# Kernel optimization log

Hardware: AMD Instinct MI355X
Metric: run time of the kernel (lower is better)

## Reference

```python
import jax, jax.numpy as jnp
import numpy as np

B = 2
T = 1024
D_MODEL = 1024
EXPAND = 2
D_INNER = D_MODEL * EXPAND  # 2048
D_STATE = 16
D_CONV = 4
DT_RANK = 64  # ceil(1024/16)


def setup_inputs() -> dict:
    key = jax.random.key(0)
    ks = jax.random.split(key, 9)
    s = 0.02
    x = jax.random.normal(ks[0], (B, T, D_MODEL), jnp.float32)
    in_proj_w = jax.random.normal(ks[1], (2 * D_INNER, D_MODEL), jnp.float32) * s
    conv_w = jax.random.normal(ks[2], (D_INNER, 1, D_CONV), jnp.float32) * 0.1
    conv_b = jax.random.normal(ks[3], (D_INNER,), jnp.float32) * 0.01
    x_proj_w = jax.random.normal(ks[4], (DT_RANK + 2 * D_STATE, D_INNER), jnp.float32) * s
    dt_proj_w = jax.random.normal(ks[5], (D_INNER, DT_RANK), jnp.float32) * s
    dt_proj_b = jax.random.uniform(ks[6], (D_INNER,), jnp.float32, -4.0, -2.0)
    A_log = jnp.log(jnp.tile(jnp.arange(1, D_STATE + 1, dtype=jnp.float32), (D_INNER, 1)))
    D_param = jnp.ones((D_INNER,), jnp.float32)
    out_proj_w = jax.random.normal(ks[7], (D_MODEL, D_INNER), jnp.float32) * s
    return {"x": x, "in_proj_w": in_proj_w, "conv_w": conv_w, "conv_b": conv_b,
            "x_proj_w": x_proj_w, "dt_proj_w": dt_proj_w, "dt_proj_b": dt_proj_b,
            "A_log": A_log, "D_param": D_param, "out_proj_w": out_proj_w}


def reference(x, in_proj_w, conv_w, conv_b, x_proj_w, dt_proj_w, dt_proj_b,
              A_log, D_param, out_proj_w):
    Bsz, Tlen, _ = x.shape
    # input projection -> (B,T,2*d_inner); split into x-branch and gate z
    xz = jnp.einsum('btd,ed->bte', x, in_proj_w)
    xs, z = jnp.split(xz, 2, axis=-1)
    # causal depthwise conv1d: torch pads both sides by d_conv-1 then slices [:T],
    # equivalent to left-pad d_conv-1
    xc = jnp.swapaxes(xs, 1, 2)  # (B, d_inner, T)
    xc = jax.lax.conv_general_dilated(xc, conv_w, window_strides=(1,),
                                      padding=[(D_CONV - 1, 0)],
                                      feature_group_count=D_INNER)
    xc = xc + conv_b[None, :, None]
    xs = jax.nn.silu(jnp.swapaxes(xc, 1, 2))  # (B,T,d_inner)
    A = -jnp.exp(A_log)  # (d_inner, d_state)
    x_dbl = jnp.einsum('bti,ei->bte', xs, x_proj_w)
    dt, Bv, Cv = jnp.split(x_dbl, [DT_RANK, DT_RANK + D_STATE], axis=-1)
    dt = jax.nn.softplus(jnp.einsum('btr,ir->bti', dt, dt_proj_w) + dt_proj_b)
    # selective scan: h_t = exp(dt_t*A)*h_{t-1} + (dt_t*x_t)*B_t ; y_t = <h_t, C_t>
    def step(h, inp):
        dt_t, B_t, C_t, x_t = inp  # (B,Di),(B,Ds),(B,Ds),(B,Di)
        dA = jnp.exp(dt_t[:, :, None] * A[None])        # (B,Di,Ds)
        h = dA * h + (dt_t * x_t)[:, :, None] * B_t[:, None, :]
        y_t = jnp.einsum('bds,bs->bd', h, C_t)
        return h, y_t
    tm = lambda a: jnp.swapaxes(a, 0, 1)  # time-major
    h0 = jnp.zeros((Bsz, D_INNER, D_STATE), x.dtype)
    _, ys = jax.lax.scan(step, h0, (tm(dt), tm(Bv), tm(Cv), tm(xs)))
    y = jnp.swapaxes(ys, 0, 1) + xs * D_param  # (B,T,d_inner)
    y = y * jax.nn.silu(z)
    return jnp.einsum('bti,di->btd', y, out_proj_w)
```

## Files before the change

kernel.cpp:

```cpp
#include <hip/hip_runtime.h>
#include <hip/hip_bf16.h>
#include <math.h>

#define B_SZ 2
#define T_LEN 1024
#define DMODEL 1024
#define DINNER 2048
#define DSTATE 16
#define DCONV 4
#define DTRANK 64
#define MTOK (B_SZ * T_LEN)

#define NC 32
#define CLEN (T_LEN / NC)
#define NCH (B_SZ * DINNER)
#define NSTATES (NCH * DSTATE)

#define XPK 8
#define XPKC (DINNER / XPK)

typedef __bf16 bf16x4 __attribute__((ext_vector_type(4)));
typedef __bf16 bf16x8 __attribute__((ext_vector_type(8)));
typedef float  f32x4  __attribute__((ext_vector_type(4)));

__device__ __forceinline__ float sigmoid_f(float v) { return 1.f / (1.f + __expf(-v)); }

__global__ __launch_bounds__(256) void convert4(const float* __restrict__ x,
                                                const float* __restrict__ w_in,
                                                const float* __restrict__ w_out,
                                                const float* __restrict__ w_xp,
                                                __bf16* __restrict__ xb,
                                                __bf16* __restrict__ wb_in,
                                                __bf16* __restrict__ wb_out,
                                                __bf16* __restrict__ wxp,
                                                float* __restrict__ xdbl)
{
    const int gi = blockIdx.x * blockDim.x + threadIdx.x;
    if (gi >= 1073152) {
        const int o = gi - 1073152;
        float4 z = make_float4(0.f, 0.f, 0.f, 0.f);
        reinterpret_cast<float4*>(xdbl)[2 * o]     = z;
        reinterpret_cast<float4*>(xdbl)[2 * o + 1] = z;
        return;
    }
    const float* src; __bf16* dst; int o;
    if (gi < 262144)       { src = x;     dst = xb;     o = gi; }
    else if (gi < 786432)  { src = w_in;  dst = wb_in;  o = gi - 262144; }
    else if (gi < 1048576) { src = w_out; dst = wb_out; o = gi - 786432; }
    else                   { src = w_xp;  dst = wxp;    o = gi - 1048576; }
    float4 a = reinterpret_cast<const float4*>(src)[2 * o];
    float4 b = reinterpret_cast<const float4*>(src)[2 * o + 1];
    bf16x8 v = {(__bf16)a.x, (__bf16)a.y, (__bf16)a.z, (__bf16)a.w,
                (__bf16)b.x, (__bf16)b.y, (__bf16)b.z, (__bf16)b.w};
    reinterpret_cast<bf16x8*>(dst)[o] = v;
}

template<int BN, typename CT>
__global__ __launch_bounds__(256) void mfma_gemm_bf16(const __bf16* __restrict__ A, int lda,
                                                      const __bf16* __restrict__ Bm, int ldb,
                                                      CT* __restrict__ C, int ldc, int K)
{
    constexpr int NF = BN / 32;
    constexpr int BCALLS = BN / 32;
    __shared__ __align__(16) __bf16 As[128 * 64];
    __shared__ __align__(16) __bf16 Bs[BN * 64];
    const int tid  = threadIdx.x;
    const int lane = tid & 63;
    const int w    = tid >> 6;
    const int wr   = w >> 1, wc = w & 1;
    const int m0   = blockIdx.y * 128, n0 = blockIdx.x * BN;

    f32x4 acc[4][NF];
    #pragma unroll
    for (int i = 0; i < 4; ++i)
        #pragma unroll
        for (int j = 0; j < NF; ++j) {
            f32x4 z = {0.f, 0.f, 0.f, 0.f};
            acc[i][j] = z;
        }

    const int fr = lane & 15;
    const int kq = (lane >> 4) * 8;

    for (int k0 = 0; k0 < K; k0 += 64) {
        #pragma unroll
        for (int c = 0; c < 4; ++c) {
            const int idx = c * 256 + tid;
            const int row = idx >> 3;
            const int kc  = (idx & 7) * 8;
            __builtin_amdgcn_global_load_lds(
                (const __attribute__((address_space(1))) unsigned int*)(A + (size_t)(m0 + row) * lda + k0 + kc),
                (__attribute__((address_space(3))) unsigned int*)(As + idx * 8),
                16, 0, 0);
        }
        #pragma unroll
        for (int c = 0; c < BCALLS; ++c) {
            const int idx = c * 256 + tid;
            const int row = idx >> 3;
            const int kc  = (idx & 7) * 8;
            __builtin_amdgcn_global_load_lds(
                (const __attribute__((address_space(1))) unsigned int*)(Bm + (size_t)(n0 + row) * ldb + k0 + kc),
                (__attribute__((address_space(3))) unsigned int*)(Bs + idx * 8),
                16, 0, 0);
        }
        __syncthreads();

        bf16x8 af[4][2], bfr[NF][2];
        #pragma unroll
        for (int i = 0; i < 4; ++i) {
            const __bf16* pa = As + (wr * 64 + i * 16 + fr) * 64 + kq;
            af[i][0] = *reinterpret_cast<const bf16x8*>(pa);
            af[i][1] = *reinterpret_cast<const bf16x8*>(pa + 32);
        }
        #pragma unroll
        for (int j = 0; j < NF; ++j) {
            const __bf16* pb = Bs + (wc * (BN / 2) + j * 16 + fr) * 64 + kq;
            bfr[j][0] = *reinterpret_cast<const bf16x8*>(pb);
            bfr[j][1] = *reinterpret_cast<const bf16x8*>(pb + 32);
        }
        #pragma unroll
        for (int i = 0; i < 4; ++i)
            #pragma unroll
            for (int j = 0; j < NF; ++j) {
                acc[i][j] = __builtin_amdgcn_mfma_f32_16x16x32_bf16(af[i][0], bfr[j][0], acc[i][j], 0, 0, 0);
                acc[i][j] = __builtin_amdgcn_mfma_f32_16x16x32_bf16(af[i][1], bfr[j][1], acc[i][j], 0, 0, 0);
            }
        __syncthreads();
    }

    const int crow = (lane >> 4) * 4;
    const int ccol = lane & 15;
    #pragma unroll
    for (int i = 0; i < 4; ++i)
        #pragma unroll
        for (int j = 0; j < NF; ++j) {
            CT* cp = C + (size_t)(m0 + wr * 64 + i * 16 + crow) * ldc
                       + n0 + wc * (BN / 2) + j * 16 + ccol;
            cp[0 * (size_t)ldc] = (CT)acc[i][j][0];
            cp[1 * (size_t)ldc] = (CT)acc[i][j][1];
            cp[2 * (size_t)ldc] = (CT)acc[i][j][2];
            cp[3 * (size_t)ldc] = (CT)acc[i][j][3];
        }
}

__global__ __launch_bounds__(256) void mfma_xproj(const __bf16* __restrict__ A,
                                                  const __bf16* __restrict__ Bm,
                                                  float* __restrict__ xdbl)
{
    __shared__ __align__(16) __bf16 As[128 * 64];
    __shared__ __align__(16) __bf16 Bs[32 * 64];
    const int tid  = threadIdx.x;
    const int lane = tid & 63;
    const int w    = tid >> 6;
    const int wr   = w >> 1, wc = w & 1;
    const int m0   = blockIdx.y * 128, n0 = blockIdx.x * 32;
    const int kbeg = blockIdx.z * XPKC;

    f32x4 acc[4];
    #pragma unroll
    for (int i = 0; i < 4; ++i) { f32x4 z = {0.f, 0.f, 0.f, 0.f}; acc[i] = z; }

    const int fr = lane & 15;
    const int kq = (lane >> 4) * 8;

    for (int k0 = kbeg; k0 < kbeg + XPKC; k0 += 64) {
        #pragma unroll
        for (int c = 0; c < 4; ++c) {
            const int idx = c * 256 + tid;
            const int row = idx >> 3;
            const int kc  = (idx & 7) * 8;
            __builtin_amdgcn_global_load_lds(
                (const __attribute__((address_space(1))) unsigned int*)(A + (size_t)(m0 + row) * DINNER + k0 + kc),
                (__attribute__((address_space(3))) unsigned int*)(As + idx * 8),
                16, 0, 0);
        }
        {
            const int row = tid >> 3;
            const int kc  = (tid & 7) * 8;
            __builtin_amdgcn_global_load_lds(
                (const __attribute__((address_space(1))) unsigned int*)(Bm + (size_t)(n0 + row) * DINNER + k0 + kc),
                (__attribute__((address_space(3))) unsigned int*)(Bs + tid * 8),
                16, 0, 0);
        }
        __syncthreads();

        bf16x8 af[4][2], bfr[2];
        #pragma unroll
        for (int i = 0; i < 4; ++i) {
            const __bf16* pa = As + (wr * 64 + i * 16 + fr) * 64 + kq;
            af[i][0] = *reinterpret_cast<const bf16x8*>(pa);
            af[i][1] = *reinterpret_cast<const bf16x8*>(pa + 32);
        }
        {
            const __bf16* pb = Bs + (wc * 16 + fr) * 64 + kq;
            bfr[0] = *reinterpret_cast<const bf16x8*>(pb);
            bfr[1] = *reinterpret_cast<const bf16x8*>(pb + 32);
        }
        #pragma unroll
        for (int i = 0; i < 4; ++i) {
            acc[i] = __builtin_amdgcn_mfma_f32_16x16x32_bf16(af[i][0], bfr[0], acc[i], 0, 0, 0);
            acc[i] = __builtin_amdgcn_mfma_f32_16x16x32_bf16(af[i][1], bfr[1], acc[i], 0, 0, 0);
        }
        __syncthreads();
    }

    const int crow = (lane >> 4) * 4;
    const int ccol = lane & 15;
    const int n = n0 + wc * 16 + ccol;
    #pragma unroll
    for (int i = 0; i < 4; ++i) {
        const int m = m0 + wr * 64 + i * 16 + crow;
        unsafeAtomicAdd(&xdbl[(size_t)(m + 0) * 96 + n], acc[i][0]);
        unsafeAtomicAdd(&xdbl[(size_t)(m + 1) * 96 + n], acc[i][1]);
        unsafeAtomicAdd(&xdbl[(size_t)(m + 2) * 96 + n], acc[i][2]);
        unsafeAtomicAdd(&xdbl[(size_t)(m + 3) * 96 + n], acc[i][3]);
    }
}

__global__ __launch_bounds__(256) void conv_silu_kernel(const __bf16* __restrict__ xzb,
                                                        const float* __restrict__ cw,
                                                        const float* __restrict__ cb,
                                                        __bf16* __restrict__ xsb)
{
    int tid = blockIdx.x * blockDim.x + threadIdx.x;
    int d = tid & (DINNER - 1);
    int t = (tid >> 11) & (T_LEN - 1);
    int b = tid >> 21;
    float acc = cb[d];
    const float4 w = *reinterpret_cast<const float4*>(&cw[d * DCONV]);
    float wv[4] = {w.x, w.y, w.z, w.w};
    #pragma unroll
    for (int j = 0; j < DCONV; ++j) {
        int tt = t - (DCONV - 1) + j;
        if (tt >= 0)
            acc = fmaf((float)xzb[((size_t)(b * T_LEN + tt)) * (2 * DINNER) + d], wv[j], acc);
    }
    xsb[tid] = (__bf16)(acc * sigmoid_f(acc));
}

__global__ __launch_bounds__(256) void gemm_dtproj(const float* __restrict__ A,
                                                   const float* __restrict__ Bm,
                                                   __bf16* __restrict__ C,
                                                   const float* __restrict__ bias)
{
    __shared__ float As[16][68];
    __shared__ float Bs[16][68];
    const int tx = threadIdx.x & 15;
    const int ty = threadIdx.x >> 4;
    const int m0 = blockIdx.y * 64;
    const int n0 = blockIdx.x * 64;
    const int lr = threadIdx.x >> 2;
    const int lc = (threadIdx.x & 3) * 4;

    float acc[4][4] = {};

    for (int k0 = 0; k0 < DTRANK; k0 += 16) {
        {
            float4 v = *reinterpret_cast<const float4*>(&A[(size_t)(m0 + lr) * 96 + k0 + lc]);
            As[lc + 0][lr] = v.x; As[lc + 1][lr] = v.y;
            As[lc + 2][lr] = v.z; As[lc + 3][lr] = v.w;
        }
        {
            float4 v = *reinterpret_cast<const float4*>(&Bm[(size_t)(n0 + lr) * DTRANK + k0 + lc]);
            Bs[lc + 0][lr] = v.x; Bs[lc + 1][lr] = v.y;
            Bs[lc + 2][lr] = v.z; Bs[lc + 3][lr] = v.w;
        }
        __syncthreads();
        #pragma unroll
        for (int kk = 0; kk < 16; ++kk) {
            float av[4], bv[4];
            #pragma unroll
            for (int i = 0; i < 4; ++i) av[i] = As[kk][ty + 16 * i];
            #pragma unroll
            for (int j = 0; j < 4; ++j) bv[j] = Bs[kk][tx + 16 * j];
            #pragma unroll
            for (int i = 0; i < 4; ++i)
                #pragma unroll
                for (int j = 0; j < 4; ++j)
                    acc[i][j] = fmaf(av[i], bv[j], acc[i][j]);
        }
        __syncthreads();
    }

    #pragma unroll
    for (int i = 0; i < 4; ++i) {
        int m = m0 + ty + 16 * i;
        #pragma unroll
        for (int j = 0; j < 4; ++j) {
            int n = n0 + tx + 16 * j;
            float v = acc[i][j] + bias[n];
            v = (v > 20.f) ? v : log1pf(__expf(v));
            C[(size_t)m * DINNER + n] = (__bf16)v;
        }
    }
}

__global__ __launch_bounds__(256) void scan_pass1(const __bf16* __restrict__ dtb,
                                                  const __bf16* __restrict__ xsb,
                                                  const float* __restrict__ xdbl,
                                                  const float* __restrict__ A_log,
                                                  float* __restrict__ Pb,
                                                  float* __restrict__ Bb)
{
    __shared__ float sB[CLEN][16];
    const int tid = threadIdx.x;
    const int g   = blockIdx.x * 256 + tid;
    const int c   = blockIdx.y;
    const int b   = g >> 11;
    const int d   = g & (DINNER - 1);
    const int m0  = b * T_LEN + c * CLEN;

    if (tid < CLEN * 4) {
        int t = tid >> 2, s4 = (tid & 3) * 4;
        *reinterpret_cast<float4*>(&sB[t][s4]) =
            *reinterpret_cast<const float4*>(&xdbl[(size_t)(m0 + t) * 96 + DTRANK + s4]);
    }
    __syncthreads();

    float a[DSTATE], h[DSTATE];
    #pragma unroll
    for (int s4 = 0; s4 < DSTATE; s4 += 4) {
        float4 v = *reinterpret_cast<const float4*>(&A_log[d * DSTATE + s4]);
        a[s4 + 0] = -__expf(v.x); a[s4 + 1] = -__expf(v.y);
        a[s4 + 2] = -__expf(v.z); a[s4 + 3] = -__expf(v.w);
        h[s4 + 0] = 0.f; h[s4 + 1] = 0.f; h[s4 + 2] = 0.f; h[s4 + 3] = 0.f;
    }

    float sumdt = 0.f;
    float dtc = (float)dtb[(size_t)m0 * DINNER + d];
    float xc  = (float)xsb[(size_t)m0 * DINNER + d];
    for (int t = 0; t < CLEN; ++t) {
        float dtn = 0.f, xn = 0.f;
        if (t + 1 < CLEN) {
            dtn = (float)dtb[(size_t)(m0 + t + 1) * DINNER + d];
            xn  = (float)xsb[(size_t)(m0 + t + 1) * DINNER + d];
        }
        sumdt += dtc;
        const float u = dtc * xc;
        #pragma unroll
        for (int s = 0; s < DSTATE; ++s) {
            const float dA = __expf(dtc * a[s]);
            h[s] = fmaf(dA, h[s], u * sB[t][s]);
        }
        dtc = dtn; xc = xn;
    }

    float* pp = Pb + ((size_t)c * NCH + g) * DSTATE;
    float* bp = Bb + ((size_t)c * NCH + g) * DSTATE;
    #pragma unroll
    for (int s4 = 0; s4 < DSTATE; s4 += 4) {
        float4 pv = {__expf(a[s4] * sumdt), __expf(a[s4 + 1] * sumdt),
                     __expf(a[s4 + 2] * sumdt), __expf(a[s4 + 3] * sumdt)};
        *reinterpret_cast<float4*>(pp + s4) = pv;
        float4 hv = {h[s4], h[s4 + 1], h[s4 + 2], h[s4 + 3]};
        *reinterpret_cast<float4*>(bp + s4) = hv;
    }
}

__global__ __launch_bounds__(256) void scan_pass2(const float* __restrict__ Pb,
                                                  float* __restrict__ Bb)
{
    const int idx = blockIdx.x * blockDim.x + threadIdx.x;
    float h = 0.f;
    #pragma unroll
    for (int c = 0; c < NC; ++c) {
        const size_t o = (size_t)c * NSTATES + idx;
        const float P  = Pb[o];
        const float Bv = Bb[o];
        Bb[o] = h;
        h = fmaf(P, h, Bv);
    }
}

__global__ __launch_bounds__(256) void scan_pass3(const __bf16* __restrict__ dtb,
                                                  const __bf16* __restrict__ xsb,
                                                  const float* __restrict__ xdbl,
                                                  const float* __restrict__ Hs,
                                                  const float* __restrict__ A_log,
                                                  const float* __restrict__ Dp,
                                                  const __bf16* __restrict__ xzb,
                                                  __bf16* __restrict__ yMb)
{
    __shared__ float sBC[CLEN][32];
    const int tid = threadIdx.x;
    const int g   = blockIdx.x * 256 + tid;
    const int c   = blockIdx.y;
    const int b   = g >> 11;
    const int d   = g & (DINNER - 1);
    const int m0  = b * T_LEN + c * CLEN;

    {
        int t = tid >> 3, col = (tid & 7) * 4;
        if (t < CLEN)
            *reinterpret_cast<float4*>(&sBC[t][col]) =
                *reinterpret_cast<const float4*>(&xdbl[(size_t)(m0 + t) * 96 + DTRANK + col]);
    }
    __syncthreads();

    float a[DSTATE], h[DSTATE];
    #pragma unroll
    for (int s4 = 0; s4 < DSTATE; s4 += 4) {
        float4 v = *reinterpret_cast<const float4*>(&A_log[d * DSTATE + s4]);
        a[s4 + 0] = -__expf(v.x); a[s4 + 1] = -__expf(v.y);
        a[s4 + 2] = -__expf(v.z); a[s4 + 3] = -__expf(v.w);
        float4 hv = *reinterpret_cast<const float4*>(
            Hs + ((size_t)c * NCH + g) * DSTATE + s4);
        h[s4 + 0] = hv.x; h[s4 + 1] = hv.y; h[s4 + 2] = hv.z; h[s4 + 3] = hv.w;
    }
    const float Dv = Dp[d];

    float dtc = (float)dtb[(size_t)m0 * DINNER + d];
    float xc  = (float)xsb[(size_t)m0 * DINNER + d];
    float zc  = (float)xzb[(size_t)m0 * (2 * DINNER) + DINNER + d];
    for (int t = 0; t < CLEN; ++t) {
        float dtn = 0.f, xn = 0.f, zn = 0.f;
        if (t + 1 < CLEN) {
            dtn = (float)dtb[(size_t)(m0 + t + 1) * DINNER + d];
            xn  = (float)xsb[(size_t)(m0 + t + 1) * DINNER + d];
            zn  = (float)xzb[(size_t)(m0 + t + 1) * (2 * DINNER) + DINNER + d];
        }
        const float u = dtc * xc;
        float y0 = 0.f, y1 = 0.f, y2 = 0.f, y3 = 0.f;
        #pragma unroll
        for (int s = 0; s < DSTATE; s += 4) {
            float dA0 = __expf(dtc * a[s + 0]);
            float dA1 = __expf(dtc * a[s + 1]);
            float dA2 = __expf(dtc * a[s + 2]);
            float dA3 = __expf(dtc * a[s + 3]);
            h[s + 0] = fmaf(dA0, h[s + 0], u * sBC[t][s + 0]);
            h[s + 1] = fmaf(dA1, h[s + 1], u * sBC[t][s + 1]);
            h[s + 2] = fmaf(dA2, h[s + 2], u * sBC[t][s + 2]);
            h[s + 3] = fmaf(dA3, h[s + 3], u * sBC[t][s + 3]);
            y0 = fmaf(h[s + 0], sBC[t][16 + s + 0], y0);
            y1 = fmaf(h[s + 1], sBC[t][16 + s + 1], y1);
            y2 = fmaf(h[s + 2], sBC[t][16 + s + 2], y2);
            y3 = fmaf(h[s + 3], sBC[t][16 + s + 3], y3);
        }
        float y = (y0 + y1) + (y2 + y3) + xc * Dv;
        const float gate = zc * sigmoid_f(zc);
        yMb[(size_t)(m0 + t) * DINNER + d] = (__bf16)(y * gate);
        dtc = dtn; xc = xn; zc = zn;
    }
}

extern "C" void kernel_launch(void* const* d_in, const int* in_sizes, int n_in,
                              void* d_out, int out_size, void* d_ws, size_t ws_size,
                              hipStream_t stream) {
    const float* x         = (const float*)d_in[0];
    const float* in_proj_w = (const float*)d_in[1];
    const float* conv_w    = (const float*)d_in[2];
    const float* conv_b    = (const float*)d_in[3];
    const float* x_proj_w  = (const float*)d_in[4];
    const float* dt_proj_w = (const float*)d_in[5];
    const float* dt_proj_b = (const float*)d_in[6];
    const float* A_log     = (const float*)d_in[7];
    const float* D_param   = (const float*)d_in[8];
    const float* out_proj_w= (const float*)d_in[9];
    float* out = (float*)d_out;

    float* ws = (float*)d_ws;
    const size_t M1 = (size_t)1024 * 1024;
    __bf16* xzb    = (__bf16*)ws;
    __bf16* xb     = (__bf16*)(ws + 4 * M1);
    __bf16* wb_in  = (__bf16*)(ws + 5 * M1);
    __bf16* wb_out = (__bf16*)(ws + 7 * M1);
    __bf16* wxp    = (__bf16*)(ws + 8 * M1);
    __bf16* xsb    = (__bf16*)(ws + 9 * M1);
    __bf16* dtb    = (__bf16*)(ws + 11 * M1);
    float*  xdbl   = ws + 13 * M1;
    float*  Pb     = ws + 14 * M1;
    float*  Bb     = ws + 16 * M1;
    __bf16* yMb    = (__bf16*)(ws + 18 * M1);

    dim3 blk(256);

    convert4<<<dim3(4288), blk, 0, stream>>>(x, in_proj_w, out_proj_w, x_proj_w,
                                             xb, wb_in, wb_out, wxp, xdbl);

    mfma_gemm_bf16<128, __bf16><<<dim3((2 * DINNER) / 128, MTOK / 128), blk, 0, stream>>>(
        xb, DMODEL, wb_in, DMODEL, xzb, 2 * DINNER, DMODEL);

    conv_silu_kernel<<<dim3(B_SZ * T_LEN * DINNER / 256), blk, 0, stream>>>(xzb, conv_w, conv_b, xsb);

    mfma_xproj<<<dim3(3, MTOK / 128, XPK), blk, 0, stream>>>(xsb, wxp, xdbl);

    gemm_dtproj<<<dim3(DINNER / 64, MTOK / 64), blk, 0, stream>>>(xdbl, dt_proj_w, dtb, dt_proj_b);

    scan_pass1<<<dim3(NCH / 256, NC), blk, 0, stream>>>(dtb, xsb, xdbl, A_log, Pb, Bb);
    scan_pass2<<<dim3(NSTATES / 256), blk, 0, stream>>>(Pb, Bb);
    scan_pass3<<<dim3(NCH / 256, NC), blk, 0, stream>>>(dtb, xsb, xdbl, Bb, A_log, D_param, xzb, yMb);

    mfma_gemm_bf16<64, float><<<dim3(DMODEL / 64, MTOK / 128), blk, 0, stream>>>(
        yMb, DINNER, wb_out, DINNER, out, DMODEL, DINNER);
}
```

Measured before the change: 177.9 us.

## Split-K out-projection with atomics, swizzle in-proj blocks, vectorize conv-SiLU

The out-projection GEMM switches to 128x128 tiles with a split-K of 2 that accumulates through float atomics. The output is zeroed in the extended conversion kernel. The in-projection GEMM gets a specialized kernel with a block-index swizzle meant to improve L2 locality. The depthwise conv+SiLU now handles 8 channels per thread with vector bf16 loads and stores. Atomics add contention and make the summation order nondeterministic. Zeroing the output adds extra writes.

```diff
diff --git a/kernel.cpp b/kernel.cpp
--- a/kernel.cpp
+++ b/kernel.cpp
@@ -25,7 +25,7 @@
 
 __device__ __forceinline__ float sigmoid_f(float v) { return 1.f / (1.f + __expf(-v)); }
 
-__global__ __launch_bounds__(256) void convert4(const float* __restrict__ x,
+__global__ __launch_bounds__(256) void convert5(const float* __restrict__ x,
                                                 const float* __restrict__ w_in,
                                                 const float* __restrict__ w_out,
                                                 const float* __restrict__ w_xp,
@@ -33,14 +33,16 @@
                                                 __bf16* __restrict__ wb_in,
                                                 __bf16* __restrict__ wb_out,
                                                 __bf16* __restrict__ wxp,
-                                                float* __restrict__ xdbl)
+                                                float* __restrict__ xdbl,
+                                                float* __restrict__ outz)
 {
     const int gi = blockIdx.x * blockDim.x + threadIdx.x;
     if (gi >= 1073152) {
-        const int o = gi - 1073152;
+        float* dst = (gi < 1097728) ? xdbl : outz;
+        const int o = (gi < 1097728) ? gi - 1073152 : gi - 1097728;
         float4 z = make_float4(0.f, 0.f, 0.f, 0.f);
-        reinterpret_cast<float4*>(xdbl)[2 * o]     = z;
-        reinterpret_cast<float4*>(xdbl)[2 * o + 1] = z;
+        reinterpret_cast<float4*>(dst)[2 * o]     = z;
+        reinterpret_cast<float4*>(dst)[2 * o + 1] = z;
         return;
     }
     const float* src; __bf16* dst; int o;
@@ -55,26 +57,27 @@
     reinterpret_cast<bf16x8*>(dst)[o] = v;
 }
 
-template<int BN, typename CT>
-__global__ __launch_bounds__(256) void mfma_gemm_bf16(const __bf16* __restrict__ A, int lda,
-                                                      const __bf16* __restrict__ Bm, int ldb,
-                                                      CT* __restrict__ C, int ldc, int K)
-{
-    constexpr int NF = BN / 32;
-    constexpr int BCALLS = BN / 32;
+__global__ __launch_bounds__(256) void mfma_inproj(const __bf16* __restrict__ A,
+                                                   const __bf16* __restrict__ Bm,
+                                                   __bf16* __restrict__ C)
+{
     __shared__ __align__(16) __bf16 As[128 * 64];
-    __shared__ __align__(16) __bf16 Bs[BN * 64];
+    __shared__ __align__(16) __bf16 Bs[128 * 64];
     const int tid  = threadIdx.x;
     const int lane = tid & 63;
     const int w    = tid >> 6;
     const int wr   = w >> 1, wc = w & 1;
-    const int m0   = blockIdx.y * 128, n0 = blockIdx.x * BN;
-
-    f32x4 acc[4][NF];
+
+    int bid = blockIdx.y * 32 + blockIdx.x;
+    bid = (bid & 7) * 64 + (bid >> 3);
+    const int m0 = (bid >> 5) * 128;
+    const int n0 = (bid & 31) * 128;
+
+    f32x4 acc[4][4];
     #pragma unroll
     for (int i = 0; i < 4; ++i)
         #pragma unroll
-        for (int j = 0; j < NF; ++j) {
+        for (int j = 0; j < 4; ++j) {
             f32x4 z = {0.f, 0.f, 0.f, 0.f};
             acc[i][j] = z;
         }
@@ -82,30 +85,104 @@
     const int fr = lane & 15;
     const int kq = (lane >> 4) * 8;
 
-    for (int k0 = 0; k0 < K; k0 += 64) {
+    for (int k0 = 0; k0 < DMODEL; k0 += 64) {
         #pragma unroll
         for (int c = 0; c < 4; ++c) {
             const int idx = c * 256 + tid;
             const int row = idx >> 3;
             const int kc  = (idx & 7) * 8;
             __builtin_amdgcn_global_load_lds(
-                (const __attribute__((address_space(1))) unsigned int*)(A + (size_t)(m0 + row) * lda + k0 + kc),
+                (const __attribute__((address_space(1))) unsigned int*)(A + (size_t)(m0 + row) * DMODEL + k0 + kc),
                 (__attribute__((address_space(3))) unsigned int*)(As + idx * 8),
                 16, 0, 0);
-        }
-        #pragma unroll
-        for (int c = 0; c < BCALLS; ++c) {
+            __builtin_amdgcn_global_load_lds(
+                (const __attribute__((address_space(1))) unsigned int*)(Bm + (size_t)(n0 + row) * DMODEL + k0 + kc),
+                (__attribute__((address_space(3))) unsigned int*)(Bs + idx * 8),
+                16, 0, 0);
+        }
+        __syncthreads();
+
+        bf16x8 af[4][2], bfr[4][2];
+        #pragma unroll
+        for (int i = 0; i < 4; ++i) {
+            const __bf16* pa = As + (wr * 64 + i * 16 + fr) * 64 + kq;
+            af[i][0] = *reinterpret_cast<const bf16x8*>(pa);
+            af[i][1] = *reinterpret_cast<const bf16x8*>(pa + 32);
+        }
+        #pragma unroll
+        for (int j = 0; j < 4; ++j) {
+            const __bf16* pb = Bs + (wc * 64 + j * 16 + fr) * 64 + kq;
+            bfr[j][0] = *reinterpret_cast<const bf16x8*>(pb);
+            bfr[j][1] = *reinterpret_cast<const bf16x8*>(pb + 32);
+        }
+        #pragma unroll
+        for (int i = 0; i < 4; ++i)
+            #pragma unroll
+            for (int j = 0; j < 4; ++j) {
+                acc[i][j] = __builtin_amdgcn_mfma_f32_16x16x32_bf16(af[i][0], bfr[j][0], acc[i][j], 0, 0, 0);
+                acc[i][j] = __builtin_amdgcn_mfma_f32_16x16x32_bf16(af[i][1], bfr[j][1], acc[i][j], 0, 0, 0);
+            }
+        __syncthreads();
+    }
+
+    const int crow = (lane >> 4) * 4;
+    const int ccol = lane & 15;
+    #pragma unroll
+    for (int i = 0; i < 4; ++i)
+        #pragma unroll
+        for (int j = 0; j < 4; ++j) {
+            __bf16* cp = C + (size_t)(m0 + wr * 64 + i * 16 + crow) * (2 * DINNER)
+                           + n0 + wc * 64 + j * 16 + ccol;
+            cp[0 * (2 * DINNER)] = (__bf16)acc[i][j][0];
+            cp[1 * (2 * DINNER)] = (__bf16)acc[i][j][1];
+            cp[2 * (2 * DINNER)] = (__bf16)acc[i][j][2];
+            cp[3 * (2 * DINNER)] = (__bf16)acc[i][j][3];
+        }
+}
+
+__global__ __launch_bounds__(256) void mfma_outproj(const __bf16* __restrict__ A,
+                                                    const __bf16* __restrict__ Bm,
+                                                    float* __restrict__ C)
+{
+    __shared__ __align__(16) __bf16 As[128 * 64];
+    __shared__ __align__(16) __bf16 Bs[128 * 64];
+    const int tid  = threadIdx.x;
+    const int lane = tid & 63;
+    const int w    = tid >> 6;
+    const int wr   = w >> 1, wc = w & 1;
+    const int m0   = blockIdx.y * 128, n0 = blockIdx.x * 128;
+    const int kbeg = blockIdx.z * (DINNER / 2);
+
+    f32x4 acc[4][4];
+    #pragma unroll
+    for (int i = 0; i < 4; ++i)
+        #pragma unroll
+        for (int j = 0; j < 4; ++j) {
+            f32x4 z = {0.f, 0.f, 0.f, 0.f};
+            acc[i][j] = z;
+        }
+
+    const int fr = lane & 15;
+    const int kq = (lane >> 4) * 8;
+
+    for (int k0 = kbeg; k0 < kbeg + DINNER / 2; k0 += 64) {
+        #pragma unroll
+        for (int c = 0; c < 4; ++c) {
             const int idx = c * 256 + tid;
             const int row = idx >> 3;
             const int kc  = (idx & 7) * 8;
             __builtin_amdgcn_global_load_lds(
-                (const __attribute__((address_space(1))) unsigned int*)(Bm + (size_t)(n0 + row) * ldb + k0 + kc),
+                (const __attribute__((address_space(1))) unsigned int*)(A + (size_t)(m0 + row) * DINNER + k0 + kc),
+                (__attribute__((address_space(3))) unsigned int*)(As + idx * 8),
+                16, 0, 0);
+            __builtin_amdgcn_global_load_lds(
+                (const __attribute__((address_space(1))) unsigned int*)(Bm + (size_t)(n0 + row) * DINNER + k0 + kc),
                 (__attribute__((address_space(3))) unsigned int*)(Bs + idx * 8),
                 16, 0, 0);
         }
         __syncthreads();
 
-        bf16x8 af[4][2], bfr[NF][2];
+        bf16x8 af[4][2], bfr[4][2];
         #pragma unroll
         for (int i = 0; i < 4; ++i) {
             const __bf16* pa = As + (wr * 64 + i * 16 + fr) * 64 + kq;
@@ -113,15 +190,15 @@
             af[i][1] = *reinterpret_cast<const bf16x8*>(pa + 32);
         }
         #pragma unroll
-        for (int j = 0; j < NF; ++j) {
-            const __bf16* pb = Bs + (wc * (BN / 2) + j * 16 + fr) * 64 + kq;
+        for (int j = 0; j < 4; ++j) {
+            const __bf16* pb = Bs + (wc * 64 + j * 16 + fr) * 64 + kq;
             bfr[j][0] = *reinterpret_cast<const bf16x8*>(pb);
             bfr[j][1] = *reinterpret_cast<const bf16x8*>(pb + 32);
         }
         #pragma unroll
         for (int i = 0; i < 4; ++i)
             #pragma unroll
-            for (int j = 0; j < NF; ++j) {
+            for (int j = 0; j < 4; ++j) {
                 acc[i][j] = __builtin_amdgcn_mfma_f32_16x16x32_bf16(af[i][0], bfr[j][0], acc[i][j], 0, 0, 0);
                 acc[i][j] = __builtin_amdgcn_mfma_f32_16x16x32_bf16(af[i][1], bfr[j][1], acc[i][j], 0, 0, 0);
             }
@@ -133,13 +210,13 @@
     #pragma unroll
     for (int i = 0; i < 4; ++i)
         #pragma unroll
-        for (int j = 0; j < NF; ++j) {
-            CT* cp = C + (size_t)(m0 + wr * 64 + i * 16 + crow) * ldc
-                       + n0 + wc * (BN / 2) + j * 16 + ccol;
-            cp[0 * (size_t)ldc] = (CT)acc[i][j][0];
-            cp[1 * (size_t)ldc] = (CT)acc[i][j][1];
-            cp[2 * (size_t)ldc] = (CT)acc[i][j][2];
-            cp[3 * (size_t)ldc] = (CT)acc[i][j][3];
+        for (int j = 0; j < 4; ++j) {
+            float* cp = C + (size_t)(m0 + wr * 64 + i * 16 + crow) * DMODEL
+                          + n0 + wc * 64 + j * 16 + ccol;
+            unsafeAtomicAdd(cp + 0 * DMODEL, acc[i][j][0]);
+            unsafeAtomicAdd(cp + 1 * DMODEL, acc[i][j][1]);
+            unsafeAtomicAdd(cp + 2 * DMODEL, acc[i][j][2]);
+            unsafeAtomicAdd(cp + 3 * DMODEL, acc[i][j][3]);
         }
 }
 
@@ -217,25 +294,54 @@
     }
 }
 
-__global__ __launch_bounds__(256) void conv_silu_kernel(const __bf16* __restrict__ xzb,
-                                                        const float* __restrict__ cw,
-                                                        const float* __restrict__ cb,
-                                                        __bf16* __restrict__ xsb)
-{
-    int tid = blockIdx.x * blockDim.x + threadIdx.x;
-    int d = tid & (DINNER - 1);
-    int t = (tid >> 11) & (T_LEN - 1);
-    int b = tid >> 21;
-    float acc = cb[d];
-    const float4 w = *reinterpret_cast<const float4*>(&cw[d * DCONV]);
-    float wv[4] = {w.x, w.y, w.z, w.w};
+__global__ __launch_bounds__(256) void conv_silu_v8(const __bf16* __restrict__ xzb,
+                                                    const float* __restrict__ cw,
+                                                    const float* __restrict__ cb,
+                                                    __bf16* __restrict__ xsb)
+{
+    const int gid = blockIdx.x * blockDim.x + threadIdx.x;
+    const int dg  = gid & (DINNER / 8 - 1);
+    const int m   = gid >> 8;
+    const int t   = m & (T_LEN - 1);
+    const int d0  = dg * 8;
+
+    float acc[8];
+    {
+        float4 b0 = *reinterpret_cast<const float4*>(&cb[d0]);
+        float4 b1 = *reinterpret_cast<const float4*>(&cb[d0 + 4]);
+        acc[0] = b0.x; acc[1] = b0.y; acc[2] = b0.z; acc[3] = b0.w;
+        acc[4] = b1.x; acc[5] = b1.y; acc[6] = b1.z; acc[7] = b1.w;
+    }
+    float4 wv[8];
+    #pragma unroll
+    for (int c = 0; c < 8; ++c)
+        wv[c] = *reinterpret_cast<const float4*>(&cw[(d0 + c) * DCONV]);
+
     #pragma unroll
     for (int j = 0; j < DCONV; ++j) {
-        int tt = t - (DCONV - 1) + j;
-        if (tt >= 0)
-            acc = fmaf((float)xzb[((size_t)(b * T_LEN + tt)) * (2 * DINNER) + d], wv[j], acc);
-    }
-    xsb[tid] = (__bf16)(acc * sigmoid_f(acc));
+        const int tt = t - (DCONV - 1) + j;
+        if (tt >= 0) {
+            bf16x8 v = *reinterpret_cast<const bf16x8*>(
+                &xzb[(size_t)(m - (DCONV - 1) + j) * (2 * DINNER) + d0]);
+            const float wj0 = (j == 0) ? 1.f : 0.f;
+            (void)wj0;
+            acc[0] = fmaf((float)v[0], (&wv[0].x)[j], acc[0]);
+            acc[1] = fmaf((float)v[1], (&wv[1].x)[j], acc[1]);
+            acc[2] = fmaf((float)v[2], (&wv[2].x)[j], acc[2]);
+            acc[3] = fmaf((float)v[3], (&wv[3].x)[j], acc[3]);
+            acc[4] = fmaf((float)v[4], (&wv[4].x)[j], acc[4]);
+            acc[5] = fmaf((float)v[5], (&wv[5].x)[j], acc[5]);
+            acc[6] = fmaf((float)v[6], (&wv[6].x)[j], acc[6]);
+            acc[7] = fmaf((float)v[7], (&wv[7].x)[j], acc[7]);
+        }
+    }
+    bf16x8 o;
+    #pragma unroll
+    for (int c = 0; c < 8; ++c) {
+        float s = acc[c] * sigmoid_f(acc[c]);
+        o[c] = (__bf16)s;
+    }
+    *reinterpret_cast<bf16x8*>(&xsb[(size_t)m * DINNER + d0]) = o;
 }
 
 __global__ __launch_bounds__(256) void gemm_dtproj(const float* __restrict__ A,
@@ -474,13 +580,12 @@
 
     dim3 blk(256);
 
-    convert4<<<dim3(4288), blk, 0, stream>>>(x, in_proj_w, out_proj_w, x_proj_w,
-                                             xb, wb_in, wb_out, wxp, xdbl);
-
-    mfma_gemm_bf16<128, __bf16><<<dim3((2 * DINNER) / 128, MTOK / 128), blk, 0, stream>>>(
-        xb, DMODEL, wb_in, DMODEL, xzb, 2 * DINNER, DMODEL);
-
-    conv_silu_kernel<<<dim3(B_SZ * T_LEN * DINNER / 256), blk, 0, stream>>>(xzb, conv_w, conv_b, xsb);
+    convert5<<<dim3(5312), blk, 0, stream>>>(x, in_proj_w, out_proj_w, x_proj_w,
+                                             xb, wb_in, wb_out, wxp, xdbl, out);
+
+    mfma_inproj<<<dim3(32, 16), blk, 0, stream>>>(xb, wb_in, xzb);
+
+    conv_silu_v8<<<dim3(MTOK * DINNER / 8 / 256), blk, 0, stream>>>(xzb, conv_w, conv_b, xsb);
 
     mfma_xproj<<<dim3(3, MTOK / 128, XPK), blk, 0, stream>>>(xsb, wxp, xdbl);
 
@@ -490,6 +595,5 @@
     scan_pass2<<<dim3(NSTATES / 256), blk, 0, stream>>>(Pb, Bb);
     scan_pass3<<<dim3(NCH / 256, NC), blk, 0, stream>>>(dtb, xsb, xdbl, Bb, A_log, D_param, xzb, yMb);
 
-    mfma_gemm_bf16<64, float><<<dim3(DMODEL / 64, MTOK / 128), blk, 0, stream>>>(
-        yMb, DINNER, wb_out, DINNER, out, DMODEL, DINNER);
-}
+    mfma_outproj<<<dim3(DMODEL / 128, MTOK / 128, 2), blk, 0, stream>>>(yMb, wb_out, out);
+}
```

Result: slower. 184.3 us (+3.6%).
